# Optimization experiments

Measured on AMD Instinct MI355X. Metric: run time of the kernel, lower is better.

## Reference

```python
import jax, jax.numpy as jnp
import numpy as np
import math

DIM = 384
HEADS = 6
HID = 32  # PositionalEncodingFourier hidden_dim
B, H, W = 16, 56, 56


def _layer_norm(x, g, b, eps=1e-6):
    mu = jnp.mean(x, axis=-1, keepdims=True)
    var = jnp.mean((x - mu) ** 2, axis=-1, keepdims=True)
    return (x - mu) * jax.lax.rsqrt(var + eps) * g + b


def _pos_encoding_fourier(Bb, Hh, Ww, w, b):
    # EdgeNeXt PositionalEncodingFourier with all-False mask: cumsum == arange+1
    scale = 2.0 * math.pi
    y_embed = jnp.arange(1, Hh + 1, dtype=jnp.float32)[:, None] / (Hh + 1e-6) * scale
    x_embed = jnp.arange(1, Ww + 1, dtype=jnp.float32)[None, :] / (Ww + 1e-6) * scale
    dim_t = 10000.0 ** (2.0 * (jnp.arange(HID) // 2).astype(jnp.float32) / HID)
    def enc(e):
        p = jnp.broadcast_to(e, (Hh, Ww))[..., None] / dim_t  # (H,W,HID)
        return jnp.stack([jnp.sin(p[..., 0::2]), jnp.cos(p[..., 1::2])], axis=-1).reshape(Hh, Ww, HID)
    pos = jnp.concatenate([enc(y_embed), enc(x_embed)], axis=-1)  # (H,W,2*HID)
    pos = pos @ w.T + b  # 1x1 conv token_projection as matmul -> (H,W,DIM)
    return jnp.broadcast_to(jnp.transpose(pos, (2, 0, 1))[None], (Bb, DIM, Hh, Ww))


def _forward(x, pos_w, pos_b, ln_g, ln_b, gamma_xca, temperature,
             qkv_w, qkv_b, proj_w, proj_b, rpb_table, conv_w,
             bn_g, bn_b, bn_mean, bn_var, gamma):
    Bb, C, Hh, Ww = x.shape
    N = Hh * Ww
    d = C // HEADS
    xt = jnp.transpose(x.reshape(Bb, C, N), (0, 2, 1))  # (B,N,C)
    pos = _pos_encoding_fourier(Bb, Hh, Ww, pos_w, pos_b)
    xt = xt + jnp.transpose(pos.reshape(Bb, C, N), (0, 2, 1))

    # relative position bias (seq_len T=2): gather (T,T,h) -> expand (h,d^2,T,T)
    # -> nearest interp x0.5 selects element (0,0) -> pixel_shuffle(d) of constant
    # channels == per-head scalar broadcast over the (d,d) channel-attention map.
    T = 2
    rel_idx = jnp.arange(T)[:, None] - jnp.arange(T)[None, :] + T - 1  # (2,2)
    rpb = rpb_table[rel_idx.reshape(-1)].reshape(T, T, HEADS)
    bias = rpb[0, 0][None, :, None, None]  # (1,heads,1,1), broadcasts over (d,d)

    # XCA: cross-covariance (channel) attention
    xn = _layer_norm(xt, ln_g, ln_b)
    qkv = (xn @ qkv_w.T + qkv_b).reshape(Bb, N, 3, HEADS, d)
    qkv = jnp.transpose(qkv, (2, 0, 3, 4, 1))  # (3,B,h,d,N)
    q, k, v = qkv[0], qkv[1], qkv[2]
    q = q / jnp.maximum(jnp.linalg.norm(q, axis=-1, keepdims=True), 1e-12)
    k = k / jnp.maximum(jnp.linalg.norm(k, axis=-1, keepdims=True), 1e-12)
    attn = jnp.einsum('bhdn,bhen->bhde', q, k) * temperature + bias  # (B,h,d,d)
    attn = jax.nn.softmax(attn, axis=-1)
    out = jnp.einsum('bhde,bhen->bhdn', attn, v)  # (B,h,d,N)
    out = jnp.transpose(out, (0, 3, 1, 2)).reshape(Bb, N, C)
    out = out @ proj_w.T + proj_b
    xt = xt + gamma_xca * out

    x2 = jnp.transpose(xt, (0, 2, 1)).reshape(Bb, C, Hh, Ww)
    # pwconv0: conv3x3 (dim->dim, expan_ration hardcoded to 1) + BN(inference) + SiLU
    xi = jax.lax.conv_general_dilated(x2, conv_w, (1, 1), [(1, 1), (1, 1)],
                                      dimension_numbers=('NCHW', 'OIHW', 'NCHW'))
    xi = (xi - bn_mean[None, :, None, None]) * jax.lax.rsqrt(bn_var + 1e-5)[None, :, None, None]
    xi = xi * bn_g[None, :, None, None] + bn_b[None, :, None, None]
    xi = xi * jax.nn.sigmoid(xi)  # SiLU
    x2 = x2 + xi

    # faithful to source: raw reshape (NOT permute) of contiguous NCHW into (B,H,W,C)
    x3 = x2.reshape(Bb, Hh, Ww, C) * gamma
    x3 = jnp.transpose(x3, (0, 3, 1, 2))
    return x + x3


def setup_inputs() -> dict:
    key = jax.random.key(0)
    ks = jax.random.split(key, 10)
    d3 = 3 * DIM
    return {
        'x': jax.random.normal(ks[0], (B, DIM, H, W), jnp.float32),
        'pos_w': jax.random.normal(ks[1], (DIM, 2 * HID), jnp.float32) * 0.05,
        'pos_b': jnp.zeros((DIM,), jnp.float32),
        'ln_g': jnp.ones((DIM,), jnp.float32),
        'ln_b': jnp.zeros((DIM,), jnp.float32),
        'gamma_xca': jax.random.normal(ks[2], (DIM,), jnp.float32) * 0.1,
        'temperature': jnp.ones((HEADS, 1, 1), jnp.float32),
        'qkv_w': jax.random.normal(ks[3], (d3, DIM), jnp.float32) * (DIM ** -0.5),
        'qkv_b': jnp.zeros((d3,), jnp.float32),
        'proj_w': jax.random.normal(ks[4], (DIM, DIM), jnp.float32) * (DIM ** -0.5),
        'proj_b': jnp.zeros((DIM,), jnp.float32),
        'rpb_table': jax.random.normal(ks[5], (3, HEADS), jnp.float32) * 0.02,
        'conv_w': jax.random.normal(ks[6], (DIM, DIM, 3, 3), jnp.float32) * 0.02,
        'bn_g': jnp.ones((DIM,), jnp.float32),
        'bn_b': jnp.zeros((DIM,), jnp.float32),
        'bn_mean': jax.random.normal(ks[7], (DIM,), jnp.float32) * 0.1,
        'bn_var': jax.random.uniform(ks[8], (DIM,), jnp.float32, 0.5, 1.5),
        'gamma': jax.random.normal(ks[9], (DIM,), jnp.float32) * 0.1,
    }


def reference(x, pos_w, pos_b, ln_g, ln_b, gamma_xca, temperature,
              qkv_w, qkv_b, proj_w, proj_b, rpb_table, conv_w,
              bn_g, bn_b, bn_mean, bn_var, gamma):
    return _forward(x, pos_w, pos_b, ln_g, ln_b, gamma_xca, temperature,
                    qkv_w, qkv_b, proj_w, proj_b, rpb_table, conv_w,
                    bn_g, bn_b, bn_mean, bn_var, gamma)
```

## Files before the change

kernel.cpp:

```cpp
#include <hip/hip_runtime.h>
#include <hip/hip_bf16.h>
#include <math.h>

#define DIM 384
#define HEADS 6
#define NN 3136
#define BB 16
#define BH (BB*HEADS)
#define HP 58
#define NP (HP*HP)

typedef __attribute__((ext_vector_type(8))) short short8;
typedef __attribute__((ext_vector_type(4))) short short4v;
typedef __attribute__((ext_vector_type(4))) float f32x4;

__device__ __forceinline__ float bf2f(unsigned short u) {
    union { unsigned int i; float f; } v; v.i = ((unsigned int)u) << 16; return v.f;
}
__device__ __forceinline__ unsigned short f2bf(float f) {
    union { float f; unsigned int i; } v; v.f = f;
    unsigned int r = v.i + 0x7fffu + ((v.i >> 16) & 1u);
    return (unsigned short)(r >> 16);
}
__device__ __forceinline__ void glds16(const unsigned short* g, void* l) {
    __builtin_amdgcn_global_load_lds(
        (const __attribute__((address_space(1))) unsigned int*)g,
        (__attribute__((address_space(3))) unsigned int*)l, 16, 0, 0);
}

__global__ void kw_convert(const float* __restrict__ qkv_w, const float* __restrict__ proj_w,
                           const float* __restrict__ conv_w,
                           unsigned short* __restrict__ Wq, unsigned short* __restrict__ Wp,
                           unsigned short* __restrict__ Wc) {
    int tid = blockIdx.x * 256 + threadIdx.x;
    int stride = gridDim.x * 256;
    for (int i = tid; i < 3*DIM*DIM; i += stride) Wq[i] = f2bf(qkv_w[i]);
    for (int i = tid; i < DIM*DIM; i += stride) Wp[i] = f2bf(proj_w[i]);
    for (int i = tid; i < DIM*DIM*9; i += stride) {
        int ii = i % DIM; int rest = i / DIM; int tap = rest % 9; int o = rest / 9;
        Wc[i] = f2bf(conv_w[(size_t)(o*DIM + ii)*9 + tap]);
    }
}

__global__ void k_pos(const float* __restrict__ pos_w, const float* __restrict__ pos_b,
                      float* __restrict__ P) {
    int n = blockIdx.x; int h = n / 56, w = n % 56;
    __shared__ float feat[64];
    int t = threadIdx.x;
    if (t < 64) {
        int axis = t >> 5;
        int k = t & 31; int i = k >> 1;
        float e = (float)((axis ? w : h) + 1) / 56.000001f * 6.28318530717958647692f;
        float arg = e / powf(10000.0f, (float)i / 16.0f);
        feat[t] = (k & 1) ? cosf(arg) : sinf(arg);
    }
    __syncthreads();
    for (int c = t; c < DIM; c += blockDim.x) {
        float s = pos_b[c];
        #pragma unroll 8
        for (int k = 0; k < 64; k++) s += feat[k] * pos_w[c*64 + k];
        P[(size_t)n*DIM + c] = s;
    }
}

__global__ __launch_bounds__(256) void k_tln(const float* __restrict__ x, const float* __restrict__ P,
                                             const float* __restrict__ g, const float* __restrict__ be,
                                             float* __restrict__ XT, unsigned short* __restrict__ XN) {
    __shared__ float tile[32][388];
    int blk = blockIdx.x;
    int b = blk / 98, nt = blk % 98;
    int n0 = nt*32;
    int t = threadIdx.x;
    #pragma unroll
    for (int it = 0; it < 12; it++) {
        int task = it*256 + t;
        int c = task >> 3, seg = task & 7;
        float4 v = *reinterpret_cast<const float4*>(x + ((size_t)(b*DIM + c))*NN + n0 + seg*4);
        tile[seg*4+0][c] = v.x; tile[seg*4+1][c] = v.y;
        tile[seg*4+2][c] = v.z; tile[seg*4+3][c] = v.w;
    }
    __syncthreads();
    int row = t >> 3, sub = t & 7;
    int n = n0 + row;
    f32x4 xp[12];
    float s = 0.f;
    #pragma unroll
    for (int k = 0; k < 12; k++) {
        int c0 = (k*8 + sub)*4;
        float4 tv = *reinterpret_cast<float4*>(&tile[row][c0]);
        float4 pv = *reinterpret_cast<const float4*>(P + (size_t)n*DIM + c0);
        f32x4 xv = {tv.x+pv.x, tv.y+pv.y, tv.z+pv.z, tv.w+pv.w};
        xp[k] = xv;
        s += xv[0]+xv[1]+xv[2]+xv[3];
        *reinterpret_cast<float4*>(XT + ((size_t)(b*NN + n))*DIM + c0) = *(float4*)&xv;
    }
    s += __shfl_xor(s, 1, 64); s += __shfl_xor(s, 2, 64); s += __shfl_xor(s, 4, 64);
    float mean = s * (1.0f/384.0f);
    float sq = 0.f;
    #pragma unroll
    for (int k = 0; k < 12; k++) {
        #pragma unroll
        for (int e = 0; e < 4; e++) { float d = xp[k][e]-mean; sq += d*d; }
    }
    sq += __shfl_xor(sq, 1, 64); sq += __shfl_xor(sq, 2, 64); sq += __shfl_xor(sq, 4, 64);
    float rs = rsqrtf(sq * (1.0f/384.0f) + 1e-6f);
    #pragma unroll
    for (int k = 0; k < 12; k++) {
        int c0 = (k*8 + sub)*4;
        unsigned short pk[4];
        #pragma unroll
        for (int e = 0; e < 4; e++)
            pk[e] = f2bf((xp[k][e]-mean)*rs*g[c0+e] + be[c0+e]);
        *reinterpret_cast<short4v*>(XN + ((size_t)(b*NN + n))*DIM + c0) = *(short4v*)pk;
    }
}

template<int MODE>
__global__ __launch_bounds__(256) void k_gemm(
    const unsigned short* __restrict__ A, const unsigned short* __restrict__ Wt,
    const float* __restrict__ bias,
    unsigned short* __restrict__ Qb, unsigned short* __restrict__ Kb, unsigned short* __restrict__ Vt,
    const float* __restrict__ XTp, const float* __restrict__ gxca, unsigned short* __restrict__ X2p)
{
    __shared__ __align__(16) char smem[35328];
    auto ctA = (float(*)[69])smem;
    auto ctB = (float(*)[130])smem;

    constexpr int NCT = (MODE == 0) ? 9 : 3;
    constexpr int CPX = (MODE == 0) ? 441 : 147;
    int bid = blockIdx.x;
    int orig = (bid & 7)*CPX + (bid >> 3);
    int ct = orig % NCT, mt = orig / NCT;
    int m0 = mt*128, o0 = ct*128;
    int t = threadIdx.x;
    int wave = t >> 6, lane = t & 63;
    int wr = wave >> 1, wc = wave & 1;
    int lr = lane & 15, lg = lane >> 4;

    int r0 = t >> 2;
    int swcol = (((t & 3) ^ ((t >> 3) & 3)) << 3);
    const unsigned short* a0 = A  + (size_t)(m0 + r0)*384 + swcol;
    const unsigned short* a1 = A  + (size_t)(m0 + 64 + r0)*384 + swcol;
    const unsigned short* b0 = Wt + (size_t)(o0 + r0)*384 + swcol;
    const unsigned short* b1 = Wt + (size_t)(o0 + 64 + r0)*384 + swcol;
    int rsw = ((lr >> 1) & 3) << 3;

    auto stage = [&](char* base, int c) {
        glds16(a0 + c, base + wave*1024);
        glds16(a1 + c, base + 4096 + wave*1024);
        glds16(b0 + c, base + 8192 + wave*1024);
        glds16(b1 + c, base + 12288 + wave*1024);
    };

    f32x4 acc[4][4];
    #pragma unroll
    for (int i=0;i<4;i++) for (int j=0;j<4;j++) acc[i][j] = (f32x4){0.f,0.f,0.f,0.f};

    stage(smem, 0);
    __syncthreads();
    for (int kk = 0; kk < 12; kk++) {
        if (kk < 11) stage(smem + ((kk+1)&1)*16384, (kk+1)*32);
        auto As = (unsigned short(*)[32])(smem + (kk&1)*16384);
        auto Bs = (unsigned short(*)[32])(smem + (kk&1)*16384 + 8192);
        short8 af[4], bfv[4];
        #pragma unroll
        for (int i=0;i<4;i++) af[i]  = *(short8*)&As[wr*64 + i*16 + lr][(lg*8) ^ rsw];
        #pragma unroll
        for (int j=0;j<4;j++) bfv[j] = *(short8*)&Bs[wc*64 + j*16 + lr][(lg*8) ^ rsw];
        #pragma unroll
        for (int i=0;i<4;i++)
            #pragma unroll
            for (int j=0;j<4;j++)
                acc[i][j] = __builtin_amdgcn_mfma_f32_16x16x32_bf16(af[i], bfv[j], acc[i][j], 0, 0, 0);
        __syncthreads();
    }

    int comp = (MODE == 0) ? (o0 / DIM) : 0;
    for (int mh = 0; mh < 2; mh++) {
        __syncthreads();
        bool useB = (MODE == 1) || (MODE == 0 && comp == 2);
        if (wr == mh) {
            if (useB) {
                #pragma unroll
                for (int i=0;i<4;i++) for (int j=0;j<4;j++) for (int r=0;r<4;r++)
                    ctB[i*16 + lg*4 + r][wc*64 + j*16 + lr] = acc[i][j][r];
            } else {
                #pragma unroll
                for (int i=0;i<4;i++) for (int j=0;j<4;j++) for (int r=0;r<4;r++)
                    ctA[wc*64 + j*16 + lr][i*16 + lg*4 + r] = acc[i][j][r];
            }
        }
        __syncthreads();
        if (MODE == 1) {
            for (int q = t; q < 1024; q += 256) {
                int row = q >> 4, seg = q & 15;
                int m = m0 + mh*64 + row; int b = m/NN; int n = m - b*NN;
                int py = n/56, px = n - py*56;
                int og0 = o0 + seg*8;
                float xv[8];
                *(float4*)xv     = *(const float4*)(XTp + (size_t)m*DIM + og0);
                *(float4*)(xv+4) = *(const float4*)(XTp + (size_t)m*DIM + og0 + 4);
                unsigned short pk[8];
                #pragma unroll
                for (int e=0;e<8;e++) {
                    float val = ctB[row][seg*8+e] + bias[og0+e];
                    pk[e] = f2bf(xv[e] + gxca[og0+e]*val);
                }
                *(short8*)(X2p + ((size_t)(b*NP + (py+1)*HP + px + 1))*DIM + og0) = *(short8*)pk;
            }
        } else if (comp < 2) {
            unsigned short* Dst = (comp == 0) ? Qb : Kb;
            for (int q = t; q < 2048; q += 256) {
                int row = q >> 4, seg = q & 15;
                int og = o0 + row; int rem = og - comp*DIM;
                int hh = rem >> 6, dd = rem & 63;
                int m4 = m0 + mh*64 + seg*4; int b = m4/NN; int n = m4 - b*NN;
                float bv = bias[og];
                unsigned short pk[4];
                #pragma unroll
                for (int e=0;e<4;e++) pk[e] = f2bf(ctA[row][seg*4+e] + bv);
                *(short4v*)(Dst + ((size_t)((b*HEADS + hh)*64 + dd))*NN + n) = *(short4v*)pk;
            }
        } else {
            for (int q = t; q < 1024; q += 256) {
                int row = q >> 4, seg = q & 15;
                int m = m0 + mh*64 + row; int b = m/NN; int n = m - b*NN;
                int og0 = o0 + seg*8; int rem0 = og0 - 2*DIM;
                int hh = rem0 >> 6, dd0 = rem0 & 63;
                unsigned short pk[8];
                #pragma unroll
                for (int e=0;e<8;e++) pk[e] = f2bf(ctB[row][seg*8+e] + bias[og0+e]);
                *(short8*)(Vt + ((size_t)((b*HEADS + hh)*NN + n))*64 + dd0) = *(short8*)pk;
            }
        }
    }
}

__global__ __launch_bounds__(256) void k_conv(
    const unsigned short* __restrict__ A, const unsigned short* __restrict__ Wt,
    const float* __restrict__ bn_g, const float* __restrict__ bn_b,
    const float* __restrict__ bn_mean, const float* __restrict__ bn_var,
    float* __restrict__ Yout)
{
    __shared__ __align__(16) char smem[32768];
    auto ctA = (float(*)[69])smem;
    auto X2s = (unsigned short(*)[68])(smem + 17664);

    int bid = blockIdx.x;
    int orig = (bid & 7)*150 + (bid >> 3);
    int ct = orig % 3; int rest = orig / 3;
    int tile = rest % 25; int b = rest / 25;
    int n0 = tile*128, o0 = ct*128;
    int t = threadIdx.x;
    int wave = t >> 6, lane = t & 63;
    int wr = wave >> 1, wc = wave & 1;
    int lr = lane & 15, lg = lane >> 4;
    int qb = n0 + 2*(n0/56);
    const size_t bbase = (size_t)b*NP*DIM;

    int swcol = (((t & 3) ^ ((t >> 3) & 3)) << 3);
    const unsigned short* asrc[4];
    #pragma unroll
    for (int j=0;j<4;j++) {
        int task = j*256 + t;
        int row = task >> 2;
        int q = qb + row; if (q > NP-1) q = NP-1;
        asrc[j] = A + bbase + (size_t)q*DIM + swcol;
    }
    const unsigned short* bsrc0 = Wt + (size_t)(o0 + (t>>2))*3456 + swcol;
    const unsigned short* bsrc1 = Wt + (size_t)(o0 + 64 + (t>>2))*3456 + swcol;

    int qrel[4];
    #pragma unroll
    for (int i=0;i<4;i++) {
        int loc = wr*64 + i*16 + lr;
        int n = n0 + loc; if (n >= NN) n = NN-1;
        qrel[i] = n + 2*(n/56) - qb;
    }

    auto stageA = [&](int c) {
        #pragma unroll
        for (int j=0;j<4;j++) glds16(asrc[j] + c, smem + j*4096 + wave*1024);
    };
    auto stageB = [&](char* base, int off) {
        glds16(bsrc0 + off, base + wave*1024);
        glds16(bsrc1 + off, base + 4096 + wave*1024);
    };

    f32x4 acc[4][4];
    #pragma unroll
    for (int i=0;i<4;i++) for (int j=0;j<4;j++) acc[i][j] = (f32x4){0.f,0.f,0.f,0.f};

    stageA(0); stageB(smem + 16384, 0);
    __syncthreads();
    for (int kk = 0; kk < 12; kk++) {
        int c = kk*32;
        auto Ah = (unsigned short(*)[32])smem;
        #pragma unroll
        for (int tap = 0; tap < 9; tap++) {
            int buf = tap & 1;
            if (tap < 8) stageB(smem + 16384 + (buf^1)*8192, (tap+1)*384 + c);
            auto Bs = (unsigned short(*)[32])(smem + 16384 + buf*8192);
            int toff = (tap/3)*58 + (tap%3);
            short8 af[4], bfv[4];
            #pragma unroll
            for (int j=0;j<4;j++)
                bfv[j] = *(short8*)&Bs[wc*64 + j*16 + lr][(lg*8) ^ (((lr>>1)&3)<<3)];
            #pragma unroll
            for (int i=0;i<4;i++) {
                int row = qrel[i] + toff;
                af[i] = *(short8*)&Ah[row][(lg*8) ^ (((row>>1)&3)<<3)];
            }
            #pragma unroll
            for (int i=0;i<4;i++)
                #pragma unroll
                for (int j=0;j<4;j++)
                    acc[i][j] = __builtin_amdgcn_mfma_f32_16x16x32_bf16(af[i], bfv[j], acc[i][j], 0, 0, 0);
            __syncthreads();
        }
        if (kk < 11) {
            stageA(c + 32);
            stageB(smem + 16384, c + 32);
            __syncthreads();
        }
    }

    for (int mh = 0; mh < 2; mh++) {
        for (int oh = 0; oh < 2; oh++) {
            __syncthreads();
            if (wr == mh && wc == oh) {
                #pragma unroll
                for (int i=0;i<4;i++) for (int j=0;j<4;j++) for (int r=0;r<4;r++)
                    ctA[j*16 + lr][i*16 + lg*4 + r] = acc[i][j][r];
            }
            for (int q = t; q < 512; q += 256) {
                int row = q >> 3, sg = q & 7;
                int n = n0 + mh*64 + row; int nc = (n < NN) ? n : NN-1;
                int qq = nc + 2*(nc/56) + 59;
                short8 v = *(const short8*)(A + bbase + (size_t)qq*DIM + o0 + oh*64 + sg*8);
                short4v lo = {v[0],v[1],v[2],v[3]}, hi = {v[4],v[5],v[6],v[7]};
                *(short4v*)&X2s[row][sg*8]     = lo;
                *(short4v*)&X2s[row][sg*8 + 4] = hi;
            }
            __syncthreads();
            for (int q = t; q < 1024; q += 256) {
                int orow = q >> 4, sg = q & 15;
                int o = o0 + oh*64 + orow;
                int n = n0 + mh*64 + sg*4;
                if (n < NN) {
                    float mean = bn_mean[o], rs = rsqrtf(bn_var[o] + 1e-5f);
                    float gg = bn_g[o], bb2 = bn_b[o];
                    float4 ov; float* po = &ov.x;
                    #pragma unroll
                    for (int e=0;e<4;e++) {
                        float xi = (ctA[orow][sg*4+e] - mean)*rs*gg + bb2;
                        float si = xi / (1.0f + __expf(-xi));
                        po[e] = si + bf2f(X2s[sg*4+e][orow]);
                    }
                    *(float4*)(Yout + ((size_t)(b*DIM + o))*NN + n) = ov;
                }
            }
        }
    }
}

__global__ __launch_bounds__(256) void k_qk(const unsigned short* __restrict__ Qb,
                                            const unsigned short* __restrict__ Kb,
                                            float* __restrict__ Gp, float* __restrict__ Np) {
    int cx = blockIdx.x, bh = blockIdx.y;
    int t = threadIdx.x, wave = t >> 6, lane = t & 63;
    int lr = lane & 15, lg = lane >> 4;
    {
        int row = t >> 1, p = t & 1;
        const unsigned short* src = (row < 64)
            ? Qb + ((size_t)bh*64 + row)*NN + cx*448
            : Kb + ((size_t)bh*64 + (row-64))*NN + cx*448;
        float s = 0.f;
        #pragma unroll
        for (int it = 0; it < 28; it++) {
            short8 v = *(const short8*)(src + p*224 + it*8);
            #pragma unroll
            for (int jj=0;jj<8;jj++) { float f = bf2f((unsigned short)v[jj]); s += f*f; }
        }
        s += __shfl_xor(s, 1, 64);
        if (p == 0) Np[((size_t)bh*7 + cx)*128 + row] = s;
    }
    f32x4 acc[4];
    #pragma unroll
    for (int j=0;j<4;j++) acc[j] = (f32x4){0.f,0.f,0.f,0.f};
    const unsigned short* qrow = Qb + ((size_t)bh*64 + wave*16 + lr)*NN + cx*448;
    const unsigned short* kbase = Kb + (size_t)bh*64*NN + cx*448;
    for (int ks = 0; ks < 14; ks++) {
        short8 a = *(const short8*)(qrow + ks*32 + lg*8);
        #pragma unroll
        for (int j=0;j<4;j++) {
            short8 bfr = *(const short8*)(kbase + (size_t)(j*16+lr)*NN + ks*32 + lg*8);
            acc[j] = __builtin_amdgcn_mfma_f32_16x16x32_bf16(a, bfr, acc[j], 0, 0, 0);
        }
    }
    float* gbase = Gp + ((size_t)bh*7 + cx)*4096;
    #pragma unroll
    for (int j=0;j<4;j++)
        #pragma unroll
        for (int r=0;r<4;r++)
            gbase[(wave*16 + lg*4 + r)*64 + j*16 + lr] = acc[j][r];
}

__global__ __launch_bounds__(256) void k_sm(const float* __restrict__ Gp, const float* __restrict__ Np,
                                            const float* __restrict__ temperature,
                                            const float* __restrict__ rpb,
                                            unsigned short* __restrict__ ATT) {
    int bh = blockIdx.x; int h = bh % HEADS;
    int t = threadIdx.x;
    __shared__ float snorm[128];
    if (t < 128) {
        float s = 0.f;
        #pragma unroll
        for (int cx=0;cx<7;cx++) s += Np[((size_t)bh*7 + cx)*128 + t];
        snorm[t] = fmaxf(sqrtf(s), 1e-12f);
    }
    __syncthreads();
    int dq = t >> 2, de0 = (t & 3) * 16;
    f32x4 g[4];
    #pragma unroll
    for (int i=0;i<4;i++) g[i] = (f32x4){0.f,0.f,0.f,0.f};
    #pragma unroll
    for (int cx=0;cx<7;cx++) {
        const float* base = Gp + ((size_t)bh*7 + cx)*4096 + dq*64 + de0;
        #pragma unroll
        for (int i=0;i<4;i++) {
            float4 v = *(const float4*)(base + i*4);
            g[i][0]+=v.x; g[i][1]+=v.y; g[i][2]+=v.z; g[i][3]+=v.w;
        }
    }
    float temp = temperature[h];
    float bias = rpb[HEADS + h];
    float qn = snorm[dq];
    float lv[16]; float mx = -1e30f;
    #pragma unroll
    for (int i=0;i<4;i++)
        #pragma unroll
        for (int e=0;e<4;e++) {
            int de = de0 + i*4 + e;
            float v = g[i][e] / (qn * snorm[64 + de]) * temp + bias;
            lv[i*4+e] = v; mx = fmaxf(mx, v);
        }
    mx = fmaxf(mx, __shfl_xor(mx, 1, 64));
    mx = fmaxf(mx, __shfl_xor(mx, 2, 64));
    float se = 0.f;
    #pragma unroll
    for (int e=0;e<16;e++) { lv[e] = __expf(lv[e]-mx); se += lv[e]; }
    se += __shfl_xor(se, 1, 64);
    se += __shfl_xor(se, 2, 64);
    float inv = 1.0f/se;
    unsigned short pk[16];
    #pragma unroll
    for (int e=0;e<16;e++) pk[e] = f2bf(lv[e]*inv);
    unsigned short* dst = ATT + ((size_t)bh*64 + dq)*64 + de0;
    *(short8*)dst       = *(short8*)pk;
    *(short8*)(dst + 8) = *(short8*)(pk + 8);
}

__global__ __launch_bounds__(256) void k_pv(const unsigned short* __restrict__ ATT,
                                            const unsigned short* __restrict__ Vt,
                                            unsigned short* __restrict__ XCA) {
    int nt = blockIdx.x, bh = blockIdx.y;
    int b = bh / HEADS, h = bh % HEADS;
    int t = threadIdx.x, wave = t >> 6, lane = t & 63;
    int lr = lane & 15, lg = lane >> 4;
    int n0 = nt*64;
    __shared__ float ctP[64][67];
    f32x4 acc[4];
    for (int i=0;i<4;i++) acc[i] = (f32x4){0.f,0.f,0.f,0.f};
    for (int ks=0; ks<2; ks++) {
        short8 bfr = *reinterpret_cast<const short8*>(Vt + ((size_t)bh*NN + n0 + wave*16 + lr)*64 + ks*32 + lg*8);
        for (int i=0;i<4;i++) {
            short8 a = *reinterpret_cast<const short8*>(ATT + ((size_t)bh*64 + i*16 + lr)*64 + ks*32 + lg*8);
            acc[i] = __builtin_amdgcn_mfma_f32_16x16x32_bf16(a, bfr, acc[i], 0, 0, 0);
        }
    }
    int nl = wave*16 + lr;
    #pragma unroll
    for (int i=0;i<4;i++)
        #pragma unroll
        for (int r=0;r<4;r++) ctP[nl][i*16 + lg*4 + r] = acc[i][r];
    __syncthreads();
    for (int q = t; q < 512; q += 256) {
        int row = q >> 3, seg = q & 7;
        unsigned short pk[8];
        #pragma unroll
        for (int e=0;e<8;e++) pk[e] = f2bf(ctP[row][seg*8+e]);
        *(short8*)(XCA + ((size_t)(b*NN + n0 + row))*DIM + h*64 + seg*8) = *(short8*)pk;
    }
}

__global__ __launch_bounds__(256) void k_final(const float* __restrict__ x, const float* __restrict__ Y,
                                               const float* __restrict__ gamma, float* __restrict__ out) {
    int i = blockIdx.x, b = blockIdx.y, kc = blockIdx.z;
    __shared__ float tile[56*193];
    int t = threadIdx.x;
    int k0 = kc*192;
    const float* ybase = Y + (size_t)b*DIM*NN + (size_t)i*21504 + k0;
    for (int q = t; q < 56*48; q += 256) {
        int j = q / 48, c4 = (q % 48) * 4;
        float4 v = *reinterpret_cast<const float4*>(ybase + (size_t)j*384 + c4);
        float* dst = &tile[j*193 + c4];
        dst[0]=v.x; dst[1]=v.y; dst[2]=v.z; dst[3]=v.w;
    }
    __syncthreads();
    for (int q = t; q < 192*56; q += 256) {
        int kl = q / 56, j = q % 56;
        int k = k0 + kl;
        size_t gi = ((size_t)(b*DIM + k))*NN + (size_t)i*56 + j;
        out[gi] = x[gi] + gamma[k] * tile[j*193 + kl];
    }
}

extern "C" void kernel_launch(void* const* d_in, const int* in_sizes, int n_in,
                              void* d_out, int out_size, void* d_ws, size_t ws_size,
                              hipStream_t stream) {
    const float* x       = (const float*)d_in[0];
    const float* pos_w   = (const float*)d_in[1];
    const float* pos_b   = (const float*)d_in[2];
    const float* ln_g    = (const float*)d_in[3];
    const float* ln_b    = (const float*)d_in[4];
    const float* gxca    = (const float*)d_in[5];
    const float* temp    = (const float*)d_in[6];
    const float* qkv_w   = (const float*)d_in[7];
    const float* qkv_b   = (const float*)d_in[8];
    const float* proj_w  = (const float*)d_in[9];
    const float* proj_b  = (const float*)d_in[10];
    const float* rpb     = (const float*)d_in[11];
    const float* conv_w  = (const float*)d_in[12];
    const float* bn_g    = (const float*)d_in[13];
    const float* bn_b    = (const float*)d_in[14];
    const float* bn_mean = (const float*)d_in[15];
    const float* bn_var  = (const float*)d_in[16];
    const float* gamma   = (const float*)d_in[17];
    float* out = (float*)d_out;
    char* ws = (char*)d_ws;

    const size_t oP   = 0;
    const size_t oXT  = oP   + 4816896;
    const size_t oXN  = oXT  + 77070336;
    const size_t oQ   = oXN  + 38535168;
    const size_t oK   = oQ   + 38535168;
    const size_t oV   = oK   + 38535168;
    const size_t oATT = oV   + 38535168;
    const size_t oWq  = oATT + 786432;
    const size_t oWp  = oWq  + 884736;
    const size_t oWc  = oWp  + 294912;

    float* P            = (float*)(ws + oP);
    float* XT           = (float*)(ws + oXT);
    float* Y            = (float*)(ws + oXT);
    unsigned short* XN  = (unsigned short*)(ws + oXN);
    float* Gp           = (float*)(ws + oXN);
    float* Np           = (float*)(ws + oXN + 11010048);
    unsigned short* XCA = (unsigned short*)(ws + oXN);
    unsigned short* Qb  = (unsigned short*)(ws + oQ);
    unsigned short* X2p = (unsigned short*)(ws + oQ);
    unsigned short* Kb  = (unsigned short*)(ws + oK);
    unsigned short* Vt  = (unsigned short*)(ws + oV);
    unsigned short* ATT = (unsigned short*)(ws + oATT);
    unsigned short* Wq  = (unsigned short*)(ws + oWq);
    unsigned short* Wp  = (unsigned short*)(ws + oWp);
    unsigned short* Wc  = (unsigned short*)(ws + oWc);

    kw_convert<<<256, 256, 0, stream>>>(qkv_w, proj_w, conv_w, Wq, Wp, Wc);
    k_pos<<<NN, 128, 0, stream>>>(pos_w, pos_b, P);
    k_tln<<<BB*98, 256, 0, stream>>>(x, P, ln_g, ln_b, XT, XN);
    k_gemm<0><<<3528, 256, 0, stream>>>(XN, Wq, qkv_b,
        Qb, Kb, Vt, nullptr, nullptr, nullptr);
    k_qk<<<dim3(7, BH), 256, 0, stream>>>(Qb, Kb, Gp, Np);
    k_sm<<<BH, 256, 0, stream>>>(Gp, Np, temp, rpb, ATT);
    hipMemsetAsync(X2p, 0, (size_t)BB*NP*DIM*2, stream);
    k_pv<<<dim3(49, BH), 256, 0, stream>>>(ATT, Vt, XCA);
    k_gemm<1><<<1176, 256, 0, stream>>>(XCA, Wp, proj_b,
        nullptr, nullptr, nullptr, XT, gxca, X2p);
    k_conv<<<1200, 256, 0, stream>>>(X2p, Wc, bn_g, bn_b, bn_mean, bn_var, Y);
    k_final<<<dim3(56, BB, 2), 256, 0, stream>>>(x, Y, gamma, out);
}
```

Baseline: 531.5 us.

## Store residual in bf16, zero only conv padding border, widen conv to 8 waves

The residual XT is now stored in bf16 instead of fp32, halving its write in the layernorm kernel and its read in the projection epilogue. The full-buffer memset of the padded conv input is replaced by a small kernel that zeroes only the one-pixel border. The 3x3 conv kernel moves to 512 threads with 8 waves, each holding a 64x32 accumulator slice, so per-wave register use drops and more waves are available to hide latency. The bf16 residual adds rounding error to the skip path.

```diff
diff --git a/kernel.cpp b/kernel.cpp
--- a/kernel.cpp
+++ b/kernel.cpp
@@ -65,7 +65,7 @@
 
 __global__ __launch_bounds__(256) void k_tln(const float* __restrict__ x, const float* __restrict__ P,
                                              const float* __restrict__ g, const float* __restrict__ be,
-                                             float* __restrict__ XT, unsigned short* __restrict__ XN) {
+                                             unsigned short* __restrict__ XTb, unsigned short* __restrict__ XN) {
     __shared__ float tile[32][388];
     int blk = blockIdx.x;
     int b = blk / 98, nt = blk % 98;
@@ -92,7 +92,10 @@
         f32x4 xv = {tv.x+pv.x, tv.y+pv.y, tv.z+pv.z, tv.w+pv.w};
         xp[k] = xv;
         s += xv[0]+xv[1]+xv[2]+xv[3];
-        *reinterpret_cast<float4*>(XT + ((size_t)(b*NN + n))*DIM + c0) = *(float4*)&xv;
+        unsigned short pkx[4];
+        #pragma unroll
+        for (int e=0;e<4;e++) pkx[e] = f2bf(xv[e]);
+        *reinterpret_cast<short4v*>(XTb + ((size_t)(b*NN + n))*DIM + c0) = *(short4v*)pkx;
     }
     s += __shfl_xor(s, 1, 64); s += __shfl_xor(s, 2, 64); s += __shfl_xor(s, 4, 64);
     float mean = s * (1.0f/384.0f);
@@ -120,7 +123,7 @@
     const unsigned short* __restrict__ A, const unsigned short* __restrict__ Wt,
     const float* __restrict__ bias,
     unsigned short* __restrict__ Qb, unsigned short* __restrict__ Kb, unsigned short* __restrict__ Vt,
-    const float* __restrict__ XTp, const float* __restrict__ gxca, unsigned short* __restrict__ X2p)
+    const unsigned short* __restrict__ XTb, const float* __restrict__ gxca, unsigned short* __restrict__ X2p)
 {
     __shared__ __align__(16) char smem[35328];
     auto ctA = (float(*)[69])smem;
@@ -197,14 +200,12 @@
                 int m = m0 + mh*64 + row; int b = m/NN; int n = m - b*NN;
                 int py = n/56, px = n - py*56;
                 int og0 = o0 + seg*8;
-                float xv[8];
-                *(float4*)xv     = *(const float4*)(XTp + (size_t)m*DIM + og0);
-                *(float4*)(xv+4) = *(const float4*)(XTp + (size_t)m*DIM + og0 + 4);
+                short8 xvb = *(const short8*)(XTb + (size_t)m*DIM + og0);
                 unsigned short pk[8];
                 #pragma unroll
                 for (int e=0;e<8;e++) {
                     float val = ctB[row][seg*8+e] + bias[og0+e];
-                    pk[e] = f2bf(xv[e] + gxca[og0+e]*val);
+                    pk[e] = f2bf(bf2f((unsigned short)xvb[e]) + gxca[og0+e]*val);
                 }
                 *(short8*)(X2p + ((size_t)(b*NP + (py+1)*HP + px + 1))*DIM + og0) = *(short8*)pk;
             }
@@ -236,7 +237,22 @@
     }
 }
 
-__global__ __launch_bounds__(256) void k_conv(
+__global__ __launch_bounds__(256) void k_pad(unsigned short* __restrict__ X2p) {
+    int b = blockIdx.x, part = blockIdx.y;
+    unsigned short* base = X2p + (size_t)b*NP*DIM;
+    short8 z = {0,0,0,0,0,0,0,0};
+    for (int task = part*256 + threadIdx.x; task < 10944; task += 2048) {
+        int pos = task / 48, seg = task - pos*48;
+        int py, px;
+        if (pos < 58)       { py = 0;  px = pos; }
+        else if (pos < 116) { py = 57; px = pos - 58; }
+        else if (pos < 172) { py = pos - 115; px = 0; }
+        else                { py = pos - 171; px = 57; }
+        *(short8*)(base + ((size_t)(py*HP + px))*DIM + seg*8) = z;
+    }
+}
+
+__global__ __launch_bounds__(512) void k_conv(
     const unsigned short* __restrict__ A, const unsigned short* __restrict__ Wt,
     const float* __restrict__ bn_g, const float* __restrict__ bn_b,
     const float* __restrict__ bn_mean, const float* __restrict__ bn_var,
@@ -253,22 +269,20 @@
     int n0 = tile*128, o0 = ct*128;
     int t = threadIdx.x;
     int wave = t >> 6, lane = t & 63;
-    int wr = wave >> 1, wc = wave & 1;
+    int wr = wave >> 2, wc = wave & 3;
     int lr = lane & 15, lg = lane >> 4;
     int qb = n0 + 2*(n0/56);
     const size_t bbase = (size_t)b*NP*DIM;
 
     int swcol = (((t & 3) ^ ((t >> 3) & 3)) << 3);
-    const unsigned short* asrc[4];
-    #pragma unroll
-    for (int j=0;j<4;j++) {
-        int task = j*256 + t;
-        int row = task >> 2;
+    const unsigned short* asrc[2];
+    #pragma unroll
+    for (int j=0;j<2;j++) {
+        int row = j*128 + (t >> 2);
         int q = qb + row; if (q > NP-1) q = NP-1;
         asrc[j] = A + bbase + (size_t)q*DIM + swcol;
     }
-    const unsigned short* bsrc0 = Wt + (size_t)(o0 + (t>>2))*3456 + swcol;
-    const unsigned short* bsrc1 = Wt + (size_t)(o0 + 64 + (t>>2))*3456 + swcol;
+    const unsigned short* bsrc = Wt + (size_t)(o0 + (t >> 2))*3456 + swcol;
 
     int qrel[4];
     #pragma unroll
@@ -280,16 +294,15 @@
 
     auto stageA = [&](int c) {
         #pragma unroll
-        for (int j=0;j<4;j++) glds16(asrc[j] + c, smem + j*4096 + wave*1024);
+        for (int j=0;j<2;j++) glds16(asrc[j] + c, smem + j*8192 + wave*1024);
     };
     auto stageB = [&](char* base, int off) {
-        glds16(bsrc0 + off, base + wave*1024);
-        glds16(bsrc1 + off, base + 4096 + wave*1024);
+        glds16(bsrc + off, base + wave*1024);
     };
 
-    f32x4 acc[4][4];
-    #pragma unroll
-    for (int i=0;i<4;i++) for (int j=0;j<4;j++) acc[i][j] = (f32x4){0.f,0.f,0.f,0.f};
+    f32x4 acc[4][2];
+    #pragma unroll
+    for (int i=0;i<4;i++) for (int j=0;j<2;j++) acc[i][j] = (f32x4){0.f,0.f,0.f,0.f};
 
     stageA(0); stageB(smem + 16384, 0);
     __syncthreads();
@@ -302,10 +315,12 @@
             if (tap < 8) stageB(smem + 16384 + (buf^1)*8192, (tap+1)*384 + c);
             auto Bs = (unsigned short(*)[32])(smem + 16384 + buf*8192);
             int toff = (tap/3)*58 + (tap%3);
-            short8 af[4], bfv[4];
+            short8 af[4], bfv[2];
             #pragma unroll
-            for (int j=0;j<4;j++)
-                bfv[j] = *(short8*)&Bs[wc*64 + j*16 + lr][(lg*8) ^ (((lr>>1)&3)<<3)];
+            for (int j=0;j<2;j++) {
+                int brow = wc*32 + j*16 + lr;
+                bfv[j] = *(short8*)&Bs[brow][(lg*8) ^ (((brow>>1)&3)<<3)];
+            }
             #pragma unroll
             for (int i=0;i<4;i++) {
                 int row = qrel[i] + toff;
@@ -314,7 +329,7 @@
             #pragma unroll
             for (int i=0;i<4;i++)
                 #pragma unroll
-                for (int j=0;j<4;j++)
+                for (int j=0;j<2;j++)
                     acc[i][j] = __builtin_amdgcn_mfma_f32_16x16x32_bf16(af[i], bfv[j], acc[i][j], 0, 0, 0);
             __syncthreads();
         }
@@ -328,13 +343,13 @@
     for (int mh = 0; mh < 2; mh++) {
         for (int oh = 0; oh < 2; oh++) {
             __syncthreads();
-            if (wr == mh && wc == oh) {
-                #pragma unroll
-                for (int i=0;i<4;i++) for (int j=0;j<4;j++) for (int r=0;r<4;r++)
-                    ctA[j*16 + lr][i*16 + lg*4 + r] = acc[i][j][r];
-            }
-            for (int q = t; q < 512; q += 256) {
-                int row = q >> 3, sg = q & 7;
+            if (wr == mh && (wc >> 1) == oh) {
+                #pragma unroll
+                for (int i=0;i<4;i++) for (int j=0;j<2;j++) for (int r=0;r<4;r++)
+                    ctA[(wc&1)*32 + j*16 + lr][i*16 + lg*4 + r] = acc[i][j][r];
+            }
+            {
+                int row = t >> 3, sg = t & 7;
                 int n = n0 + mh*64 + row; int nc = (n < NN) ? n : NN-1;
                 int qq = nc + 2*(nc/56) + 59;
                 short8 v = *(const short8*)(A + bbase + (size_t)qq*DIM + o0 + oh*64 + sg*8);
@@ -343,7 +358,7 @@
                 *(short4v*)&X2s[row][sg*8 + 4] = hi;
             }
             __syncthreads();
-            for (int q = t; q < 1024; q += 256) {
+            for (int q = t; q < 1024; q += 512) {
                 int orow = q >> 4, sg = q & 15;
                 int o = o0 + oh*64 + orow;
                 int n = n0 + mh*64 + sg*4;
@@ -552,7 +567,7 @@
     const size_t oWc  = oWp  + 294912;
 
     float* P            = (float*)(ws + oP);
-    float* XT           = (float*)(ws + oXT);
+    unsigned short* XTb = (unsigned short*)(ws + oXT);
     float* Y            = (float*)(ws + oXT);
     unsigned short* XN  = (unsigned short*)(ws + oXN);
     float* Gp           = (float*)(ws + oXN);
@@ -569,15 +584,15 @@
 
     kw_convert<<<256, 256, 0, stream>>>(qkv_w, proj_w, conv_w, Wq, Wp, Wc);
     k_pos<<<NN, 128, 0, stream>>>(pos_w, pos_b, P);
-    k_tln<<<BB*98, 256, 0, stream>>>(x, P, ln_g, ln_b, XT, XN);
+    k_tln<<<BB*98, 256, 0, stream>>>(x, P, ln_g, ln_b, XTb, XN);
     k_gemm<0><<<3528, 256, 0, stream>>>(XN, Wq, qkv_b,
         Qb, Kb, Vt, nullptr, nullptr, nullptr);
     k_qk<<<dim3(7, BH), 256, 0, stream>>>(Qb, Kb, Gp, Np);
     k_sm<<<BH, 256, 0, stream>>>(Gp, Np, temp, rpb, ATT);
-    hipMemsetAsync(X2p, 0, (size_t)BB*NP*DIM*2, stream);
+    k_pad<<<dim3(BB, 8), 256, 0, stream>>>(X2p);
     k_pv<<<dim3(49, BH), 256, 0, stream>>>(ATT, Vt, XCA);
     k_gemm<1><<<1176, 256, 0, stream>>>(XCA, Wp, proj_b,
-        nullptr, nullptr, nullptr, XT, gxca, X2p);
-    k_conv<<<1200, 256, 0, stream>>>(X2p, Wc, bn_g, bn_b, bn_mean, bn_var, Y);
+        nullptr, nullptr, nullptr, XTb, gxca, X2p);
+    k_conv<<<1200, 512, 0, stream>>>(X2p, Wc, bn_g, bn_b, bn_mean, bn_var, Y);
     k_final<<<dim3(56, BB, 2), 256, 0, stream>>>(x, Y, gamma, out);
 }
```

After: 505.8 us. -4.8%, faster.
